# Performance work log

Measured on AMD Instinct MI355X. Metric: run time of the kernel, lower is better.

Reference implementation:

```python
import jax, jax.numpy as jnp
import numpy as np

NEG_SLOPE = 0.2  # PyG GATConv default LeakyReLU slope


def _gat_conv(x, edge_index, W, a_src, a_dst, bias, heads, out_dim, concat):
    """PyG-style GATConv (eval mode, add_self_loops=True).
    x: [N, F_in], edge_index: [2, E] (row=src, col=dst)."""
    N = x.shape[0]
    loops = jnp.tile(jnp.arange(N, dtype=edge_index.dtype)[None, :], (2, 1))
    ei = jnp.concatenate([edge_index, loops], axis=1)  # [2, E+N]
    src, dst = ei[0], ei[1]

    h = (x @ W).reshape(N, heads, out_dim)            # [N, H, D]
    alpha_s = jnp.einsum('nhd,hd->nh', h, a_src)       # [N, H]
    alpha_d = jnp.einsum('nhd,hd->nh', h, a_dst)       # [N, H]

    e = jax.nn.leaky_relu(alpha_s[src] + alpha_d[dst], NEG_SLOPE)  # [E', H]
    # segment softmax over edges grouped by destination node
    m = jax.ops.segment_max(e, dst, num_segments=N)
    e = jnp.exp(e - jax.lax.stop_gradient(m)[dst])
    denom = jax.ops.segment_sum(e, dst, num_segments=N)
    alpha = e / denom[dst]                              # [E', H]

    msg = h[src] * alpha[..., None]                     # [E', H, D]
    out = jax.ops.segment_sum(msg, dst, num_segments=N) # [N, H, D]
    out = out.reshape(N, heads * out_dim) if concat else out.mean(axis=1)
    return out + bias


def setup_inputs() -> dict:
    key = jax.random.key(0)
    ks = jax.random.split(key, 12)
    N, E, F_in, H, D = 50000, 1600000, 64, 2, 32
    s = 0.1
    return {
        'x': jax.random.normal(ks[0], (N, F_in), jnp.float32),
        'edge_index': jax.random.randint(ks[1], (2, E), 0, N, jnp.int64 if jax.config.jax_enable_x64 else jnp.int32),
        'W1': jax.random.normal(ks[2], (F_in, H * D), jnp.float32) * s,
        'a_src1': jax.random.normal(ks[3], (H, D), jnp.float32) * s,
        'a_dst1': jax.random.normal(ks[4], (H, D), jnp.float32) * s,
        'b1': jnp.zeros((H * D,), jnp.float32),
        'W2': jax.random.normal(ks[5], (H * D, D), jnp.float32) * s,
        'a_src2': jax.random.normal(ks[6], (1, D), jnp.float32) * s,
        'a_dst2': jax.random.normal(ks[7], (1, D), jnp.float32) * s,
        'b2': jnp.zeros((D,), jnp.float32),
        'fcW': jax.random.normal(ks[8], (D, 1), jnp.float32) * s,
        'fcb': jnp.zeros((1,), jnp.float32),
    }


def reference(x, edge_index, W1, a_src1, a_dst1, b1, W2, a_src2, a_dst2, b2, fcW, fcb):
    H, D = 2, 32
    h = _gat_conv(x, edge_index, W1, a_src1, a_dst1, b1, heads=H, out_dim=D, concat=True)
    h = jax.nn.elu(h)
    # dropout p=0.1 is a no-op in eval mode
    h = _gat_conv(h, edge_index, W2, a_src2, a_dst2, b2, heads=1, out_dim=D, concat=False)
    h = jax.nn.elu(h)
    scores = h @ fcW + fcb
    return (scores, h)
```

## Files before the change

### kernel.cpp

```cpp
#include <hip/hip_runtime.h>
#include <hip/hip_fp16.h>

#define NEG_SLOPE 0.2f
#define NRANGE 8
#define CAP 96

__device__ __forceinline__ float elu_f(float x) {
    return x > 0.f ? x : __expf(x) - 1.f;
}
__device__ __forceinline__ float lrelu_f(float x) {
    return fmaxf(x, NEG_SLOPE * x);
}

union H4 { float2 f2; __half2 h2[2]; };

__global__ __launch_bounds__(256) void scat_gemm1_kernel(
    const int* __restrict__ ei, int* __restrict__ cnt,
    unsigned short* __restrict__ srclist, int E, int N,
    int nScat, int nChunks,
    const float* __restrict__ x, const float* __restrict__ W1,
    const float* __restrict__ a_src, const float* __restrict__ a_dst,
    __half* __restrict__ h1, float* __restrict__ as1, float* __restrict__ ad1)
{
    __shared__ float Xl[4][64];
    int b = blockIdx.x;
    if (b < 7 * nScat && (b % 7) == 0) {
        int hid = b / 7;
        int range = hid & (NRANGE - 1);
        int chunk = hid >> 3;
        int RS = (N + NRANGE - 1) / NRANGE;
        int lo = range * RS;
        unsigned span = (unsigned)(((lo + RS) > N ? N : (lo + RS)) - lo);
        int per = (((E + nChunks - 1) / nChunks) + 7) & ~7;
        int beg = chunk * per;
        int end = beg + per; if (end > E) end = E;
        if (beg >= E) return;

        int nfull = (end - beg) >> 11;
        for (int j = 0; j < nfull; ++j) {
            int i = beg + (j << 11) + (int)threadIdx.x * 8;
            int4 d0 = *(const int4*)(ei + E + i);
            int4 d1 = *(const int4*)(ei + E + i + 4);
            int4 s0 = *(const int4*)(ei + i);
            int4 s1 = *(const int4*)(ei + i + 4);
            int ds[8] = { d0.x, d0.y, d0.z, d0.w, d1.x, d1.y, d1.z, d1.w };
            int ss[8] = { s0.x, s0.y, s0.z, s0.w, s1.x, s1.y, s1.z, s1.w };
            int pos[8];
            bool pr[8];
#pragma unroll
            for (int k = 0; k < 8; ++k) {
                pr[k] = (unsigned)(ds[k] - lo) < span;
                if (pr[k]) pos[k] = atomicAdd(&cnt[ds[k]], 1);
            }
#pragma unroll
            for (int k = 0; k < 8; ++k) {
                if (pr[k])
                    srclist[(size_t)ds[k] * CAP + pos[k]] =
                        (unsigned short)ss[k];
            }
        }
        for (int i = beg + (nfull << 11) + (int)threadIdx.x; i < end; i += 256) {
            int dst = ei[E + i];
            if ((unsigned)(dst - lo) < span) {
                int src = ei[i];
                int pos = atomicAdd(&cnt[dst], 1);
                srclist[(size_t)dst * CAP + pos] = (unsigned short)src;
            }
        }
        return;
    }
    int gid = (b < 7 * nScat) ? (b - b / 7 - 1) : (b - nScat);
    int tid = threadIdx.x;
    int r   = tid >> 6;
    int col = tid & 63;
    int row = gid * 4 + r;
    if (row < N) Xl[r][col] = x[(size_t)row * 64 + col];
    __syncthreads();
    if (row >= N) return;

    float acc = 0.f;
#pragma unroll
    for (int k = 0; k < 64; ++k) acc += Xl[r][k] * W1[k * 64 + col];
    h1[(size_t)row * 64 + col] = __float2half(acc);

    int head = col >> 5;
    float ps = acc * a_src[col];
    float pd = acc * a_dst[col];
#pragma unroll
    for (int off = 16; off; off >>= 1) {
        ps += __shfl_xor(ps, off, 32);
        pd += __shfl_xor(pd, off, 32);
    }
    if ((col & 31) == 0) {
        as1[row * 2 + head] = ps;
        ad1[row * 2 + head] = pd;
    }
}

__global__ __launch_bounds__(256) void agg1_gemm2_kernel(
    const int* __restrict__ dcnt, const unsigned short* __restrict__ srclist,
    const __half* __restrict__ h1, const float* __restrict__ as1,
    const float* __restrict__ ad1, const float* __restrict__ b1,
    const float* __restrict__ W2, const float* __restrict__ a_s2,
    const float* __restrict__ a_d2,
    __half* __restrict__ h2, float* __restrict__ as2, float* __restrict__ ad2,
    int N)
{
    __shared__ float W2l[64 * 32];
    __shared__ float sh[4][64];
    int tid = threadIdx.x;
    for (int i = tid; i < 64 * 32; i += 256) W2l[i] = W2[i];
    __syncthreads();

    int lane = tid & 63;
    int wid = tid >> 6;
    int grp = lane >> 4;
    int cl  = lane & 15;
    int head = cl >> 3;
    const __half* h1q = h1 + 4 * cl;

    for (int g = 0; g < 4; ++g) {
        int n = (blockIdx.x * 4 + g) * 4 + wid;
        if (n >= N) continue;
        float adn = ad1[n * 2 + head];

        float den = 0.f, a0 = 0.f, a1 = 0.f, a2 = 0.f, a3 = 0.f;
        int beg = n * CAP;
        int deg = dcnt[n];
        int total = deg + 1;

        for (int base = 0; base < total; base += 64) {
            int rem = total - base;
            int cnt = rem > 64 ? 64 : rem;
            int li = base + lane;
            int es = (li < deg) ? (int)srclist[beg + li] : n;
            int j = 0;
            for (; j + 8 <= cnt; j += 8) {
                int sA = __shfl(es, j + grp, 64);
                int sB = __shfl(es, j + 4 + grp, 64);
                float aA = as1[sA * 2 + head];
                float aB = as1[sB * 2 + head];
                H4 uA, uB;
                uA.f2 = *(const float2*)(h1q + (size_t)sA * 64);
                uB.f2 = *(const float2*)(h1q + (size_t)sB * 64);
                float wA = __expf(lrelu_f(aA + adn));
                float wB = __expf(lrelu_f(aB + adn));
                float2 gA01 = __half22float2(uA.h2[0]);
                float2 gA23 = __half22float2(uA.h2[1]);
                float2 gB01 = __half22float2(uB.h2[0]);
                float2 gB23 = __half22float2(uB.h2[1]);
                den += wA + wB;
                a0 += wA * gA01.x + wB * gB01.x;
                a1 += wA * gA01.y + wB * gB01.y;
                a2 += wA * gA23.x + wB * gB23.x;
                a3 += wA * gA23.y + wB * gB23.y;
            }
            for (; j < cnt; j += 4) {
                int e = j + grp;
                int s = __shfl(es, e & 63, 64);
                float a = as1[s * 2 + head];
                H4 u;
                u.f2 = *(const float2*)(h1q + (size_t)s * 64);
                float w = (e < rem) ? __expf(lrelu_f(a + adn)) : 0.f;
                float2 g01 = __half22float2(u.h2[0]);
                float2 g23 = __half22float2(u.h2[1]);
                den += w;
                a0 += w * g01.x; a1 += w * g01.y;
                a2 += w * g23.x; a3 += w * g23.y;
            }
        }
        a0 += __shfl_xor(a0, 16, 64); a1 += __shfl_xor(a1, 16, 64);
        a2 += __shfl_xor(a2, 16, 64); a3 += __shfl_xor(a3, 16, 64);
        den += __shfl_xor(den, 16, 64);
        a0 += __shfl_xor(a0, 32, 64); a1 += __shfl_xor(a1, 32, 64);
        a2 += __shfl_xor(a2, 32, 64); a3 += __shfl_xor(a3, 32, 64);
        den += __shfl_xor(den, 32, 64);

        float4 bb = *(const float4*)(b1 + 4 * cl);
        float inv = 1.f / den;
        float v0 = elu_f(a0 * inv + bb.x);
        float v1 = elu_f(a1 * inv + bb.y);
        float v2 = elu_f(a2 * inv + bb.z);
        float v3 = elu_f(a3 * inv + bb.w);
        if (grp == 0) ((float4*)sh[wid])[cl] = make_float4(v0, v1, v2, v3);

        int col = lane & 31;
        int kbase = (lane >> 5) * 32;
        float p = 0.f;
#pragma unroll
        for (int jj = 0; jj < 32; ++jj)
            p += sh[wid][kbase + jj] * W2l[(kbase + jj) * 32 + col];
        p += __shfl_xor(p, 32, 64);

        if (lane < 32) h2[(size_t)n * 32 + lane] = __float2half(p);

        float ps = p * a_s2[col];
        float pd = p * a_d2[col];
#pragma unroll
        for (int off = 16; off; off >>= 1) {
            ps += __shfl_xor(ps, off, 32);
            pd += __shfl_xor(pd, off, 32);
        }
        if (lane == 0) { as2[n] = ps; ad2[n] = pd; }
    }
}

__global__ __launch_bounds__(256) void agg2_kernel(
    const int* __restrict__ dcnt, const unsigned short* __restrict__ srclist,
    const __half* __restrict__ h2, const float* __restrict__ as2,
    const float* __restrict__ ad2, const float* __restrict__ b2,
    const float* __restrict__ fcW, const float* __restrict__ fcb,
    float* __restrict__ out, int N)
{
    int g = blockIdx.x * 256 + threadIdx.x;
    int n = g >> 5;
    if (n >= N) return;
    int l32 = g & 31;
    int grp = l32 >> 3;
    int cl  = l32 & 7;
    float adn = ad2[n];
    const __half* h2q = h2 + 4 * cl;

    float den = 0.f, a0 = 0.f, a1 = 0.f, a2 = 0.f, a3 = 0.f;
    int beg = n * CAP;
    int deg = dcnt[n];
    int total = deg + 1;

    for (int base = 0; base < total; base += 32) {
        int rem = total - base;
        int cnt = rem > 32 ? 32 : rem;
        int li = base + l32;
        int es = (li < deg) ? (int)srclist[beg + li] : n;
        int j = 0;
        for (; j + 8 <= cnt; j += 8) {
            int sA = __shfl(es, j + grp, 32);
            int sB = __shfl(es, j + 4 + grp, 32);
            float aA = as2[sA];
            float aB = as2[sB];
            H4 uA, uB;
            uA.f2 = *(const float2*)(h2q + (size_t)sA * 32);
            uB.f2 = *(const float2*)(h2q + (size_t)sB * 32);
            float wA = __expf(lrelu_f(aA + adn));
            float wB = __expf(lrelu_f(aB + adn));
            float2 gA01 = __half22float2(uA.h2[0]);
            float2 gA23 = __half22float2(uA.h2[1]);
            float2 gB01 = __half22float2(uB.h2[0]);
            float2 gB23 = __half22float2(uB.h2[1]);
            den += wA + wB;
            a0 += wA * gA01.x + wB * gB01.x;
            a1 += wA * gA01.y + wB * gB01.y;
            a2 += wA * gA23.x + wB * gB23.x;
            a3 += wA * gA23.y + wB * gB23.y;
        }
        for (; j < cnt; j += 4) {
            int e = j + grp;
            int s = __shfl(es, e & 31, 32);
            float a = as2[s];
            H4 u;
            u.f2 = *(const float2*)(h2q + (size_t)s * 32);
            float w = (e < rem) ? __expf(lrelu_f(a + adn)) : 0.f;
            float2 g01 = __half22float2(u.h2[0]);
            float2 g23 = __half22float2(u.h2[1]);
            den += w;
            a0 += w * g01.x; a1 += w * g01.y;
            a2 += w * g23.x; a3 += w * g23.y;
        }
    }
    a0 += __shfl_xor(a0, 8, 64);  a1 += __shfl_xor(a1, 8, 64);
    a2 += __shfl_xor(a2, 8, 64);  a3 += __shfl_xor(a3, 8, 64);
    den += __shfl_xor(den, 8, 64);
    a0 += __shfl_xor(a0, 16, 64); a1 += __shfl_xor(a1, 16, 64);
    a2 += __shfl_xor(a2, 16, 64); a3 += __shfl_xor(a3, 16, 64);
    den += __shfl_xor(den, 16, 64);

    float4 bb = *(const float4*)(b2 + 4 * cl);
    float inv = 1.f / den;
    float v0 = elu_f(a0 * inv + bb.x);
    float v1 = elu_f(a1 * inv + bb.y);
    float v2 = elu_f(a2 * inv + bb.z);
    float v3 = elu_f(a3 * inv + bb.w);
    if (grp == 0)
        ((float4*)(out + (size_t)N + (size_t)n * 32))[cl] =
            make_float4(v0, v1, v2, v3);

    float4 fw = *(const float4*)(fcW + 4 * cl);
    float p = v0 * fw.x + v1 * fw.y + v2 * fw.z + v3 * fw.w;
    p += __shfl_xor(p, 1, 64);
    p += __shfl_xor(p, 2, 64);
    p += __shfl_xor(p, 4, 64);
    if (l32 == 0) out[n] = p + fcb[0];
}

extern "C" void kernel_launch(void* const* d_in, const int* in_sizes, int n_in,
                              void* d_out, int out_size, void* d_ws, size_t ws_size,
                              hipStream_t stream) {
    const float* x    = (const float*)d_in[0];
    const int*   ei   = (const int*)d_in[1];
    const float* W1   = (const float*)d_in[2];
    const float* a_s1 = (const float*)d_in[3];
    const float* a_d1 = (const float*)d_in[4];
    const float* b1   = (const float*)d_in[5];
    const float* W2   = (const float*)d_in[6];
    const float* a_s2 = (const float*)d_in[7];
    const float* a_d2 = (const float*)d_in[8];
    const float* b2   = (const float*)d_in[9];
    const float* fcW  = (const float*)d_in[10];
    const float* fcb  = (const float*)d_in[11];

    const int N = in_sizes[0] / 64;
    const int E = in_sizes[1] / 2;

    float* fws  = (float*)d_ws;
    float* as1  = fws;
    float* ad1  = as1 + (size_t)2 * N;
    float* as2  = ad1 + (size_t)2 * N;
    float* ad2  = as2 + (size_t)N;
    __half* h2  = (__half*)(ad2 + (size_t)N);
    __half* h1  = h2 + (size_t)32 * N;
    int*   cnt  = (int*)(h1 + (size_t)64 * N);
    unsigned short* srclist = (unsigned short*)(cnt + N);

    hipMemsetAsync(cnt, 0, sizeof(int) * (size_t)N, stream);

    const int nChunks = 256;
    const int nScat = nChunks * NRANGE;
    const int nG1 = (N + 3) / 4;
    int extra = nG1 - 6 * nScat; if (extra < 0) extra = 0;
    scat_gemm1_kernel<<<7 * nScat + extra, 256, 0, stream>>>(
        ei, cnt, srclist, E, N, nScat, nChunks, x, W1, a_s1, a_d1, h1, as1, ad1);

    agg1_gemm2_kernel<<<((size_t)N + 15) / 16, 256, 0, stream>>>(
        cnt, srclist, h1, as1, ad1, b1, W2, a_s2, a_d2, h2, as2, ad2, N);

    agg2_kernel<<<((size_t)N * 32 + 255) / 256, 256, 0, stream>>>(
        cnt, srclist, h2, as2, ad2, b2, fcW, fcb, (float*)d_out, N);
}
```

Measured before the change: 250.5 us.

## Compute edge attention weights once per lane, shuffle them, and re-balance scatter/GEMM blocks

In both aggregation kernels, each lane now computes the attention weight for one edge once and broadcasts it with shuffles, rather than every column group recomputing exp per gathered edge. The gather loop is widened to four edges per step, and the denominator comes from a full wave reduction. The first aggregation kernel is changed from four nodes per wave in a loop to one node per wave with more blocks, and the scatter phase uses fewer dst ranges with a wider interleave against GEMM1 blocks. This trades extra shuffles and masked tail lanes for less redundant transcendental work, more memory-level parallelism, and better block balance.

Measured after the change: 240.7 us. -3.9%, faster.

```diff
diff --git a/kernel.cpp b/kernel.cpp
--- a/kernel.cpp
+++ b/kernel.cpp
@@ -2,7 +2,8 @@
 #include <hip/hip_fp16.h>
 
 #define NEG_SLOPE 0.2f
-#define NRANGE 8
+#define NRANGE 4
+#define ILV 13
 #define CAP 96
 
 __device__ __forceinline__ float elu_f(float x) {
@@ -24,10 +25,10 @@
 {
     __shared__ float Xl[4][64];
     int b = blockIdx.x;
-    if (b < 7 * nScat && (b % 7) == 0) {
-        int hid = b / 7;
+    if (b < ILV * nScat && (b % ILV) == 0) {
+        int hid = b / ILV;
         int range = hid & (NRANGE - 1);
-        int chunk = hid >> 3;
+        int chunk = hid >> 2;
         int RS = (N + NRANGE - 1) / NRANGE;
         int lo = range * RS;
         unsigned span = (unsigned)(((lo + RS) > N ? N : (lo + RS)) - lo);
@@ -69,7 +70,7 @@
         }
         return;
     }
-    int gid = (b < 7 * nScat) ? (b - b / 7 - 1) : (b - nScat);
+    int gid = (b < ILV * nScat) ? (b - b / ILV - 1) : (b - nScat);
     int tid = threadIdx.x;
     int r   = tid >> 6;
     int col = tid & 63;
@@ -112,97 +113,105 @@
     for (int i = tid; i < 64 * 32; i += 256) W2l[i] = W2[i];
     __syncthreads();
 
+    int n = (blockIdx.x * 256 + tid) >> 6;
     int lane = tid & 63;
     int wid = tid >> 6;
+    if (n >= N) return;
+
     int grp = lane >> 4;
     int cl  = lane & 15;
     int head = cl >> 3;
     const __half* h1q = h1 + 4 * cl;
-
-    for (int g = 0; g < 4; ++g) {
-        int n = (blockIdx.x * 4 + g) * 4 + wid;
-        if (n >= N) continue;
-        float adn = ad1[n * 2 + head];
-
-        float den = 0.f, a0 = 0.f, a1 = 0.f, a2 = 0.f, a3 = 0.f;
-        int beg = n * CAP;
-        int deg = dcnt[n];
-        int total = deg + 1;
-
-        for (int base = 0; base < total; base += 64) {
-            int rem = total - base;
-            int cnt = rem > 64 ? 64 : rem;
-            int li = base + lane;
-            int es = (li < deg) ? (int)srclist[beg + li] : n;
-            int j = 0;
-            for (; j + 8 <= cnt; j += 8) {
-                int sA = __shfl(es, j + grp, 64);
-                int sB = __shfl(es, j + 4 + grp, 64);
-                float aA = as1[sA * 2 + head];
-                float aB = as1[sB * 2 + head];
-                H4 uA, uB;
-                uA.f2 = *(const float2*)(h1q + (size_t)sA * 64);
-                uB.f2 = *(const float2*)(h1q + (size_t)sB * 64);
-                float wA = __expf(lrelu_f(aA + adn));
-                float wB = __expf(lrelu_f(aB + adn));
-                float2 gA01 = __half22float2(uA.h2[0]);
-                float2 gA23 = __half22float2(uA.h2[1]);
-                float2 gB01 = __half22float2(uB.h2[0]);
-                float2 gB23 = __half22float2(uB.h2[1]);
-                den += wA + wB;
-                a0 += wA * gA01.x + wB * gB01.x;
-                a1 += wA * gA01.y + wB * gB01.y;
-                a2 += wA * gA23.x + wB * gB23.x;
-                a3 += wA * gA23.y + wB * gB23.y;
-            }
-            for (; j < cnt; j += 4) {
-                int e = j + grp;
-                int s = __shfl(es, e & 63, 64);
-                float a = as1[s * 2 + head];
-                H4 u;
-                u.f2 = *(const float2*)(h1q + (size_t)s * 64);
-                float w = (e < rem) ? __expf(lrelu_f(a + adn)) : 0.f;
-                float2 g01 = __half22float2(u.h2[0]);
-                float2 g23 = __half22float2(u.h2[1]);
-                den += w;
-                a0 += w * g01.x; a1 += w * g01.y;
-                a2 += w * g23.x; a3 += w * g23.y;
-            }
-        }
-        a0 += __shfl_xor(a0, 16, 64); a1 += __shfl_xor(a1, 16, 64);
-        a2 += __shfl_xor(a2, 16, 64); a3 += __shfl_xor(a3, 16, 64);
-        den += __shfl_xor(den, 16, 64);
-        a0 += __shfl_xor(a0, 32, 64); a1 += __shfl_xor(a1, 32, 64);
-        a2 += __shfl_xor(a2, 32, 64); a3 += __shfl_xor(a3, 32, 64);
-        den += __shfl_xor(den, 32, 64);
-
-        float4 bb = *(const float4*)(b1 + 4 * cl);
-        float inv = 1.f / den;
-        float v0 = elu_f(a0 * inv + bb.x);
-        float v1 = elu_f(a1 * inv + bb.y);
-        float v2 = elu_f(a2 * inv + bb.z);
-        float v3 = elu_f(a3 * inv + bb.w);
-        if (grp == 0) ((float4*)sh[wid])[cl] = make_float4(v0, v1, v2, v3);
-
-        int col = lane & 31;
-        int kbase = (lane >> 5) * 32;
-        float p = 0.f;
-#pragma unroll
-        for (int jj = 0; jj < 32; ++jj)
-            p += sh[wid][kbase + jj] * W2l[(kbase + jj) * 32 + col];
-        p += __shfl_xor(p, 32, 64);
-
-        if (lane < 32) h2[(size_t)n * 32 + lane] = __float2half(p);
-
-        float ps = p * a_s2[col];
-        float pd = p * a_d2[col];
-#pragma unroll
-        for (int off = 16; off; off >>= 1) {
-            ps += __shfl_xor(ps, off, 32);
-            pd += __shfl_xor(pd, off, 32);
-        }
-        if (lane == 0) { as2[n] = ps; ad2[n] = pd; }
-    }
+    float2 adp = *(const float2*)(ad1 + (size_t)n * 2);
+
+    float den0 = 0.f, den1 = 0.f;
+    float a0 = 0.f, a1 = 0.f, a2 = 0.f, a3 = 0.f;
+    int beg = n * CAP;
+    int deg = dcnt[n];
+    int total = deg + 1;
+
+    for (int base = 0; base < total; base += 64) {
+        int li = base + lane;
+        int es = (li < deg) ? (int)srclist[beg + li] : n;
+        float2 asp = *(const float2*)(as1 + (size_t)es * 2);
+        float w0 = 0.f, w1 = 0.f;
+        if (li < total) {
+            w0 = __expf(lrelu_f(asp.x + adp.x));
+            w1 = __expf(lrelu_f(asp.y + adp.y));
+        }
+        den0 += w0; den1 += w1;
+
+        int cnt = total - base; if (cnt > 64) cnt = 64;
+        for (int j = 0; j < cnt; j += 16) {
+            int e0 = j + grp, e1 = j + 4 + grp, e2 = j + 8 + grp, e3 = j + 12 + grp;
+            int sA = __shfl(es, e0, 64);
+            int sB = __shfl(es, e1, 64);
+            int sC = __shfl(es, e2, 64);
+            int sD = __shfl(es, e3, 64);
+            float wA0 = __shfl(w0, e0, 64), wA1 = __shfl(w1, e0, 64);
+            float wB0 = __shfl(w0, e1, 64), wB1 = __shfl(w1, e1, 64);
+            float wC0 = __shfl(w0, e2, 64), wC1 = __shfl(w1, e2, 64);
+            float wD0 = __shfl(w0, e3, 64), wD1 = __shfl(w1, e3, 64);
+            float wA = head ? wA1 : wA0;
+            float wB = head ? wB1 : wB0;
+            float wC = head ? wC1 : wC0;
+            float wD = head ? wD1 : wD0;
+            H4 uA, uB, uC, uD;
+            uA.f2 = *(const float2*)(h1q + (size_t)sA * 64);
+            uB.f2 = *(const float2*)(h1q + (size_t)sB * 64);
+            uC.f2 = *(const float2*)(h1q + (size_t)sC * 64);
+            uD.f2 = *(const float2*)(h1q + (size_t)sD * 64);
+            float2 gA01 = __half22float2(uA.h2[0]);
+            float2 gA23 = __half22float2(uA.h2[1]);
+            float2 gB01 = __half22float2(uB.h2[0]);
+            float2 gB23 = __half22float2(uB.h2[1]);
+            float2 gC01 = __half22float2(uC.h2[0]);
+            float2 gC23 = __half22float2(uC.h2[1]);
+            float2 gD01 = __half22float2(uD.h2[0]);
+            float2 gD23 = __half22float2(uD.h2[1]);
+            a0 += wA * gA01.x + wB * gB01.x + wC * gC01.x + wD * gD01.x;
+            a1 += wA * gA01.y + wB * gB01.y + wC * gC01.y + wD * gD01.y;
+            a2 += wA * gA23.x + wB * gB23.x + wC * gC23.x + wD * gD23.x;
+            a3 += wA * gA23.y + wB * gB23.y + wC * gC23.y + wD * gD23.y;
+        }
+    }
+    a0 += __shfl_xor(a0, 16, 64); a1 += __shfl_xor(a1, 16, 64);
+    a2 += __shfl_xor(a2, 16, 64); a3 += __shfl_xor(a3, 16, 64);
+    a0 += __shfl_xor(a0, 32, 64); a1 += __shfl_xor(a1, 32, 64);
+    a2 += __shfl_xor(a2, 32, 64); a3 += __shfl_xor(a3, 32, 64);
+#pragma unroll
+    for (int off = 1; off < 64; off <<= 1) {
+        den0 += __shfl_xor(den0, off, 64);
+        den1 += __shfl_xor(den1, off, 64);
+    }
+    float den = head ? den1 : den0;
+
+    float4 bb = *(const float4*)(b1 + 4 * cl);
+    float inv = 1.f / den;
+    float v0 = elu_f(a0 * inv + bb.x);
+    float v1 = elu_f(a1 * inv + bb.y);
+    float v2 = elu_f(a2 * inv + bb.z);
+    float v3 = elu_f(a3 * inv + bb.w);
+    if (grp == 0) ((float4*)sh[wid])[cl] = make_float4(v0, v1, v2, v3);
+
+    int col = lane & 31;
+    int kbase = (lane >> 5) * 32;
+    float p = 0.f;
+#pragma unroll
+    for (int jj = 0; jj < 32; ++jj)
+        p += sh[wid][kbase + jj] * W2l[(kbase + jj) * 32 + col];
+    p += __shfl_xor(p, 32, 64);
+
+    if (lane < 32) h2[(size_t)n * 32 + lane] = __float2half(p);
+
+    float ps = p * a_s2[col];
+    float pd = p * a_d2[col];
+#pragma unroll
+    for (int off = 16; off; off >>= 1) {
+        ps += __shfl_xor(ps, off, 32);
+        pd += __shfl_xor(pd, off, 32);
+    }
+    if (lane == 0) { as2[n] = ps; ad2[n] = pd; }
 }
 
 __global__ __launch_bounds__(256) void agg2_kernel(
@@ -221,57 +230,57 @@
     float adn = ad2[n];
     const __half* h2q = h2 + 4 * cl;
 
-    float den = 0.f, a0 = 0.f, a1 = 0.f, a2 = 0.f, a3 = 0.f;
+    float denp = 0.f, a0 = 0.f, a1 = 0.f, a2 = 0.f, a3 = 0.f;
     int beg = n * CAP;
     int deg = dcnt[n];
     int total = deg + 1;
 
     for (int base = 0; base < total; base += 32) {
-        int rem = total - base;
-        int cnt = rem > 32 ? 32 : rem;
         int li = base + l32;
         int es = (li < deg) ? (int)srclist[beg + li] : n;
-        int j = 0;
-        for (; j + 8 <= cnt; j += 8) {
-            int sA = __shfl(es, j + grp, 32);
-            int sB = __shfl(es, j + 4 + grp, 32);
-            float aA = as2[sA];
-            float aB = as2[sB];
-            H4 uA, uB;
+        float asv = as2[es];
+        float w = 0.f;
+        if (li < total) w = __expf(lrelu_f(asv + adn));
+        denp += w;
+
+        int cnt = total - base; if (cnt > 32) cnt = 32;
+        for (int j = 0; j < cnt; j += 16) {
+            int e0 = j + grp, e1 = j + 4 + grp, e2 = j + 8 + grp, e3 = j + 12 + grp;
+            int sA = __shfl(es, e0, 32);
+            int sB = __shfl(es, e1, 32);
+            int sC = __shfl(es, e2, 32);
+            int sD = __shfl(es, e3, 32);
+            float wA = __shfl(w, e0, 32);
+            float wB = __shfl(w, e1, 32);
+            float wC = __shfl(w, e2, 32);
+            float wD = __shfl(w, e3, 32);
+            H4 uA, uB, uC, uD;
             uA.f2 = *(const float2*)(h2q + (size_t)sA * 32);
             uB.f2 = *(const float2*)(h2q + (size_t)sB * 32);
-            float wA = __expf(lrelu_f(aA + adn));
-            float wB = __expf(lrelu_f(aB + adn));
+            uC.f2 = *(const float2*)(h2q + (size_t)sC * 32);
+            uD.f2 = *(const float2*)(h2q + (size_t)sD * 32);
             float2 gA01 = __half22float2(uA.h2[0]);
             float2 gA23 = __half22float2(uA.h2[1]);
             float2 gB01 = __half22float2(uB.h2[0]);
             float2 gB23 = __half22float2(uB.h2[1]);
-            den += wA + wB;
-            a0 += wA * gA01.x + wB * gB01.x;
-            a1 += wA * gA01.y + wB * gB01.y;
-            a2 += wA * gA23.x + wB * gB23.x;
-            a3 += wA * gA23.y + wB * gB23.y;
-        }
-        for (; j < cnt; j += 4) {
-            int e = j + grp;
-            int s = __shfl(es, e & 31, 32);
-            float a = as2[s];
-            H4 u;
-            u.f2 = *(const float2*)(h2q + (size_t)s * 32);
-            float w = (e < rem) ? __expf(lrelu_f(a + adn)) : 0.f;
-            float2 g01 = __half22float2(u.h2[0]);
-            float2 g23 = __half22float2(u.h2[1]);
-            den += w;
-            a0 += w * g01.x; a1 += w * g01.y;
-            a2 += w * g23.x; a3 += w * g23.y;
+            float2 gC01 = __half22float2(uC.h2[0]);
+            float2 gC23 = __half22float2(uC.h2[1]);
+            float2 gD01 = __half22float2(uD.h2[0]);
+            float2 gD23 = __half22float2(uD.h2[1]);
+            a0 += wA * gA01.x + wB * gB01.x + wC * gC01.x + wD * gD01.x;
+            a1 += wA * gA01.y + wB * gB01.y + wC * gC01.y + wD * gD01.y;
+            a2 += wA * gA23.x + wB * gB23.x + wC * gC23.x + wD * gD23.x;
+            a3 += wA * gA23.y + wB * gB23.y + wC * gC23.y + wD * gD23.y;
         }
     }
     a0 += __shfl_xor(a0, 8, 64);  a1 += __shfl_xor(a1, 8, 64);
     a2 += __shfl_xor(a2, 8, 64);  a3 += __shfl_xor(a3, 8, 64);
-    den += __shfl_xor(den, 8, 64);
     a0 += __shfl_xor(a0, 16, 64); a1 += __shfl_xor(a1, 16, 64);
     a2 += __shfl_xor(a2, 16, 64); a3 += __shfl_xor(a3, 16, 64);
-    den += __shfl_xor(den, 16, 64);
+#pragma unroll
+    for (int off = 1; off < 32; off <<= 1)
+        denp += __shfl_xor(denp, off, 64);
+    float den = denp;
 
     float4 bb = *(const float4*)(b2 + 4 * cl);
     float inv = 1.f / den;
@@ -325,11 +334,11 @@
     const int nChunks = 256;
     const int nScat = nChunks * NRANGE;
     const int nG1 = (N + 3) / 4;
-    int extra = nG1 - 6 * nScat; if (extra < 0) extra = 0;
-    scat_gemm1_kernel<<<7 * nScat + extra, 256, 0, stream>>>(
+    int extra = nG1 - (ILV - 1) * nScat; if (extra < 0) extra = 0;
+    scat_gemm1_kernel<<<ILV * nScat + extra, 256, 0, stream>>>(
         ei, cnt, srclist, E, N, nScat, nChunks, x, W1, a_s1, a_d1, h1, as1, ad1);
 
-    agg1_gemm2_kernel<<<((size_t)N + 15) / 16, 256, 0, stream>>>(
+    agg1_gemm2_kernel<<<((size_t)N * 64 + 255) / 256, 256, 0, stream>>>(
         cnt, srclist, h1, as1, ad1, b1, W2, a_s2, a_d2, h2, as2, ad2, N);
 
     agg2_kernel<<<((size_t)N * 32 + 255) / 256, 256, 0, stream>>>(
```
